# Performance work log

Hardware: AMD Instinct MI355X
Metric: run time of the kernel (lower is better)

Reference implementation:

```python
import jax, jax.numpy as jnp
import numpy as np

L, H, C, V, BLK = 6, 16, 1024, 32000, 2048
B, T, TA = 2, 512, 512
DFF = 4 * C
STD = 0.02
PROJ_STD = 0.02 / np.sqrt(2 * L)  # c_proj init per module
SCALE = 1.0 / np.sqrt(C // H)


def setup_inputs() -> dict:
    key = jax.random.key(0)
    ks = iter(jax.random.split(key, 64))
    nrm = lambda shape, std=STD: jax.random.normal(next(ks), shape, jnp.float32) * std
    inp = {
        'idx': jax.random.randint(next(ks), (B, T), 0, V),
        'xa': jax.random.normal(next(ks), (B, TA, C), jnp.float32),
        'wte': nrm((V, C)),            # tied with lm_head
        'wpe': nrm((BLK, C)),
        'ln1_w': jnp.ones((L, C)), 'ln1_b': jnp.zeros((L, C)),
        'sa_wq': nrm((L, C, C)), 'sa_bq': jnp.zeros((L, C)),
        'sa_wk': nrm((L, C, C)), 'sa_bk': jnp.zeros((L, C)),
        'sa_wv': nrm((L, C, C)), 'sa_bv': jnp.zeros((L, C)),
        'sa_wo': nrm((L, C, C), PROJ_STD), 'sa_bo': jnp.zeros((L, C)),
        'ca_wq': nrm((L, C, C)), 'ca_bq': jnp.zeros((L, C)),
        'ca_wk': nrm((L, C, C)), 'ca_bk': jnp.zeros((L, C)),
        'ca_wv': nrm((L, C, C)), 'ca_bv': jnp.zeros((L, C)),
        'ca_wo': nrm((L, C, C), PROJ_STD), 'ca_bo': jnp.zeros((L, C)),
        'ln2_w': jnp.ones((L, C)), 'ln2_b': jnp.zeros((L, C)),
        'fc_w': nrm((L, C, DFF)), 'fc_b': jnp.zeros((L, DFF)),
        'pr_w': nrm((L, DFF, C), PROJ_STD), 'pr_b': jnp.zeros((L, C)),
        'lnf_w': jnp.ones((C,)), 'lnf_b': jnp.zeros((C,)),
    }
    return inp


def _ln(h, w, b):
    m = h.mean(-1, keepdims=True)
    v = jnp.mean((h - m) ** 2, -1, keepdims=True)
    return (h - m) * jax.lax.rsqrt(v + 1e-5) * w + b


def _gelu(h):  # new_gelu (tanh approximation)
    return 0.5 * h * (1.0 + jnp.tanh(np.sqrt(2.0 / np.pi) * (h + 0.044715 * h ** 3)))


def _attn(hq, hkv, wq, bq, wk, bk, wv, bv, wo, bo):
    # NB: the original applies a tril causal mask even for cross-attention.
    Bq, Tq, _ = hq.shape
    Tk = hkv.shape[1]
    D = C // H
    q = (hq @ wq + bq).reshape(Bq, Tq, H, D)
    k = (hkv @ wk + bk).reshape(Bq, Tk, H, D)
    v = (hkv @ wv + bv).reshape(Bq, Tk, H, D)
    att = jnp.einsum('bqhd,bkhd->bhqk', q, k) * SCALE
    mask = jnp.tril(jnp.ones((Tq, Tk), bool))
    att = jnp.where(mask, att, -jnp.inf)
    att = jax.nn.softmax(att, axis=-1)
    y = jnp.einsum('bhqk,bkhd->bqhd', att, v).reshape(Bq, Tq, C)
    return y @ wo + bo


def _forward(idx, xa, wte, wpe, ln1_w, ln1_b, sa_wq, sa_bq, sa_wk, sa_bk, sa_wv, sa_bv, sa_wo, sa_bo,
             ca_wq, ca_bq, ca_wk, ca_bk, ca_wv, ca_bv, ca_wo, ca_bo,
             ln2_w, ln2_b, fc_w, fc_b, pr_w, pr_b, lnf_w, lnf_b):
    t = idx.shape[1]
    x = wte[idx] + wpe[:t][None]  # [B,T,C]

    def block(h, p):
        (l1w, l1b, sqw, sqb, skw, skb, svw, svb, sow, sob,
         cqw, cqb, ckw, ckb, cvw, cvb, cow, cob,
         l2w, l2b, fw, fb, pw, pb) = p
        n = _ln(h, l1w, l1b)
        h = h + _attn(n, n, sqw, sqb, skw, skb, svw, svb, sow, sob)
        n = _ln(h, l1w, l1b)  # ln_1 reused for cross-attn, as in source
        h = h + _attn(n, xa, cqw, cqb, ckw, ckb, cvw, cvb, cow, cob)
        n = _ln(h, l2w, l2b)
        h = h + (_gelu(n @ fw + fb) @ pw + pb)
        return h, None

    xs = (ln1_w, ln1_b, sa_wq, sa_bq, sa_wk, sa_bk, sa_wv, sa_bv, sa_wo, sa_bo,
          ca_wq, ca_bq, ca_wk, ca_bk, ca_wv, ca_bv, ca_wo, ca_bo,
          ln2_w, ln2_b, fc_w, fc_b, pr_w, pr_b)
    x, _ = jax.lax.scan(block, x, xs)
    x = _ln(x, lnf_w, lnf_b)
    return x @ wte.T  # tied lm_head, [B,T,V]


def reference(idx, xa, wte, wpe, ln1_w, ln1_b, sa_wq, sa_bq, sa_wk, sa_bk, sa_wv, sa_bv, sa_wo, sa_bo,
              ca_wq, ca_bq, ca_wk, ca_bk, ca_wv, ca_bv, ca_wo, ca_bo,
              ln2_w, ln2_b, fc_w, fc_b, pr_w, pr_b, lnf_w, lnf_b):
    return _forward(idx, xa, wte, wpe, ln1_w, ln1_b, sa_wq, sa_bq, sa_wk, sa_bk, sa_wv, sa_bv, sa_wo, sa_bo,
                    ca_wq, ca_bq, ca_wk, ca_bk, ca_wv, ca_bv, ca_wo, ca_bo,
                    ln2_w, ln2_b, fc_w, fc_b, pr_w, pr_b, lnf_w, lnf_b)
```

## Files before the change

kernel.cpp:

```cpp
#include <hip/hip_runtime.h>
#include <math.h>

#define CC   1024
#define HH   16
#define DH   64
#define TT   512
#define NTOK 1024
#define DFF_ 4096
#define VV   32000
#define QKSCALE 0.125f

typedef unsigned short u16;
typedef __attribute__((ext_vector_type(8))) short short8;
typedef __attribute__((ext_vector_type(4))) float f32x4;

__device__ __forceinline__ u16 f2bf(float f) {
  union { float f; unsigned u; } v; v.f = f;
  unsigned r = v.u + 0x7FFFu + ((v.u >> 16) & 1u);
  return (u16)(r >> 16);
}
__device__ __forceinline__ float gelu_f(float h) {
  return 0.5f * h * (1.0f + tanhf(0.7978845608028654f * (h + 0.044715f * h * h * h)));
}

template <int N> __device__ __forceinline__ void waitcnt_vm() {
  if constexpr (N == 0) asm volatile("s_waitcnt vmcnt(0)" ::: "memory");
  else if constexpr (N == 1) asm volatile("s_waitcnt vmcnt(1)" ::: "memory");
  else if constexpr (N == 2) asm volatile("s_waitcnt vmcnt(2)" ::: "memory");
  else if constexpr (N == 3) asm volatile("s_waitcnt vmcnt(3)" ::: "memory");
  else if constexpr (N == 4) asm volatile("s_waitcnt vmcnt(4)" ::: "memory");
  else if constexpr (N == 5) asm volatile("s_waitcnt vmcnt(5)" ::: "memory");
  else if constexpr (N == 6) asm volatile("s_waitcnt vmcnt(6)" ::: "memory");
  else if constexpr (N == 7) asm volatile("s_waitcnt vmcnt(7)" ::: "memory");
  else if constexpr (N == 8) asm volatile("s_waitcnt vmcnt(8)" ::: "memory");
  else static_assert(N <= 8, "unsupported vmcnt");
}

#define GLD16(gp, lp) __builtin_amdgcn_global_load_lds( \
    (const __attribute__((address_space(1))) void*)(gp), \
    (__attribute__((address_space(3))) void*)(lp), 16, 0, 0)

#define MFMA(a, b, c) __builtin_amdgcn_mfma_f32_16x16x32_bf16(a, b, c, 0, 0, 0)

__global__ __launch_bounds__(256) void embed_kernel(
    const int* __restrict__ idx, const float* __restrict__ wte,
    const float* __restrict__ wpe, float* __restrict__ x) {
  int row = blockIdx.x;
  int t = row & (TT - 1);
  int id = idx[row];
  const float4* a = (const float4*)(wte + (size_t)id * CC);
  const float4* p = (const float4*)(wpe + (size_t)t * CC);
  float4* o = (float4*)(x + (size_t)row * CC);
  int c = threadIdx.x;
  float4 va = a[c], vp = p[c];
  float4 ov;
  ov.x = va.x + vp.x; ov.y = va.y + vp.y; ov.z = va.z + vp.z; ov.w = va.w + vp.w;
  o[c] = ov;
}

__global__ __launch_bounds__(256) void ln_kernel(
    const float* __restrict__ x, const float* __restrict__ w,
    const float* __restrict__ b, u16* __restrict__ out) {
  int row = blockIdx.x, tid = threadIdx.x;
  float4 v = ((const float4*)(x + (size_t)row * CC))[tid];
  float s  = v.x + v.y + v.z + v.w;
  float sq = fmaf(v.x, v.x, fmaf(v.y, v.y, fmaf(v.z, v.z, v.w * v.w)));
  for (int o = 32; o > 0; o >>= 1) { s += __shfl_down(s, o); sq += __shfl_down(sq, o); }
  __shared__ float rs[4], rq[4];
  int wid = tid >> 6, lane = tid & 63;
  if (lane == 0) { rs[wid] = s; rq[wid] = sq; }
  __syncthreads();
  s  = rs[0] + rs[1] + rs[2] + rs[3];
  sq = rq[0] + rq[1] + rq[2] + rq[3];
  float mean = s * (1.0f / CC);
  float var  = sq * (1.0f / CC) - mean * mean;
  float rstd = 1.0f / sqrtf(var + 1e-5f);
  float4 wv = ((const float4*)w)[tid];
  float4 bv = ((const float4*)b)[tid];
  ushort4 o;
  o.x = f2bf((v.x - mean) * rstd * wv.x + bv.x);
  o.y = f2bf((v.y - mean) * rstd * wv.y + bv.y);
  o.z = f2bf((v.z - mean) * rstd * wv.z + bv.z);
  o.w = f2bf((v.w - mean) * rstd * wv.w + bv.w);
  ((ushort4*)(out + (size_t)row * CC))[tid] = o;
}

__global__ __launch_bounds__(256) void wtransL_kernel(
    const float* __restrict__ w0, const float* __restrict__ w1,
    const float* __restrict__ w2, const float* __restrict__ w3,
    const float* __restrict__ w4, const float* __restrict__ w5,
    const float* __restrict__ w6, const float* __restrict__ w7,
    const float* __restrict__ fc, const float* __restrict__ pr,
    u16* __restrict__ wt, size_t dls, int lbase) {
  const size_t M1 = 1048576;
  int z = blockIdx.z;
  int l = lbase + (z >> 4), slot = z & 15;
  size_t wofs = (size_t)l * M1;
  size_t mofs = (size_t)l * 4 * M1;
  const float* src;
  size_t doff = (size_t)(l - lbase) * dls;
  int sstr, dstr;
  if (slot < 8) {
    const float* base = slot == 0 ? w0 : slot == 1 ? w1 : slot == 2 ? w2
                      : slot == 3 ? w3 : slot == 4 ? w4 : slot == 5 ? w5
                      : slot == 6 ? w6 : w7;
    src = base + wofs; sstr = 1024; doff += (size_t)slot * M1; dstr = 1024;
  } else if (slot < 12) {
    int s = slot - 8;
    src = fc + mofs + (size_t)s * 1024; sstr = 4096;
    doff += 8 * M1 + (size_t)s * M1; dstr = 1024;
  } else {
    int s = slot - 12;
    src = pr + mofs + (size_t)s * M1; sstr = 1024;
    doff += 12 * M1 + (size_t)s * 1024; dstr = 4096;
  }
  __shared__ float t[64][65];
  int bx = blockIdx.x * 64, by = blockIdx.y * 64;
  int tid = threadIdx.x;
  int r16 = tid >> 4;
  int c4  = (tid & 15) * 4;
#pragma unroll
  for (int i = 0; i < 4; ++i) {
    int row = r16 + i * 16;
    float4 v = *(const float4*)&src[(size_t)(by + row) * sstr + bx + c4];
    t[row][c4] = v.x; t[row][c4 + 1] = v.y; t[row][c4 + 2] = v.z; t[row][c4 + 3] = v.w;
  }
  __syncthreads();
#pragma unroll
  for (int i = 0; i < 4; ++i) {
    int orow = r16 + i * 16;
    ushort4 o;
    o.x = f2bf(t[c4 + 0][orow]);
    o.y = f2bf(t[c4 + 1][orow]);
    o.z = f2bf(t[c4 + 2][orow]);
    o.w = f2bf(t[c4 + 3][orow]);
    *(ushort4*)&wt[doff + (size_t)(bx + orow) * dstr + by + c4] = o;
  }
}

__global__ __launch_bounds__(256) void convbf_kernel(
    const float* __restrict__ in, u16* __restrict__ out, int n4) {
  int i = blockIdx.x * 256 + threadIdx.x;
  if (i < n4) {
    float4 v = ((const float4*)in)[i];
    ushort4 o; o.x = f2bf(v.x); o.y = f2bf(v.y); o.z = f2bf(v.z); o.w = f2bf(v.w);
    ((ushort4*)out)[i] = o;
  }
}

template <int EPI, int MODE, int BM, int BN, int BK, int SK>
__global__ __launch_bounds__(256) void gemm_bf16_kernel(
    const u16* __restrict__ A, const u16* __restrict__ A2,
    const u16* __restrict__ B, const u16* __restrict__ B2,
    const float* __restrict__ bias, const float* __restrict__ bias2,
    const float* __restrict__ bias3, float* __restrict__ Cm,
    int K, int ldc, int whichbase) {
  constexpr int WM = BM / 2, WN = BN / 2, MF = WM / 16, NF = WN / 16;
  constexpr int KS = BK / 32;
  constexpr int NB = BK / 8;
  constexpr int PA = BM * BK / 2048;
  constexpr int PB = BN * BK / 2048;
  constexpr int RPP = 2048 / BK;
  constexpr int NBUF = (MODE == 2) ? 2 : 3;
  __shared__ u16 As[NBUF][BM * BK];
  __shared__ u16 Bs[NBUF][BN * BK];
  int tid = threadIdx.x;
  int lane = tid & 63, wave = tid >> 6;
  int wr = wave >> 1, wc = wave & 1;
  int row0, col0;
  bool isq = true;
  const u16* Ause = A;
  const u16* Buse = B;
  if (MODE == 2) {
    int id = blockIdx.x;
    int wg = (id & 7) * 250 + (id >> 3);
    row0 = (wg & 7) * BM;
    col0 = (wg >> 3) * BN;
  } else if (MODE == 3) {
    int bx = blockIdx.x;
    isq = bx < (1024 / BN);
    Ause = isq ? A : A2;
    Buse = isq ? B : B2;
    col0 = (isq ? bx : bx - 1024 / BN) * BN;
    row0 = blockIdx.y * BM;
  } else {
    row0 = blockIdx.y * BM;
    col0 = blockIdx.x * BN;
  }
  const int split = (SK > 1) ? blockIdx.z : 0;
  const int Kloc = K / SK;
  const int kbase = split * Kloc;
  f32x4 acc[MF][NF];
#pragma unroll
  for (int m = 0; m < MF; ++m)
#pragma unroll
    for (int n = 0; n < NF; ++n) acc[m][n] = (f32x4){0.f, 0.f, 0.f, 0.f};

  int srow = tid / NB;
  int sblk = (BK == 64) ? ((tid & 7) ^ ((tid >> 3) & 7))
                        : ((tid & 3) ^ ((tid >> 3) & 3));
  const u16* Ab = Ause + (size_t)row0 * K + kbase;
  int arow = wr * WM + (lane & 15);
  int brow = wc * WN + (lane & 15);
  int g8 = lane >> 4;
  const int NT = Kloc / BK;

  auto compute = [&](const u16* Ac, const u16* Bc) {
#pragma unroll
    for (int ks = 0; ks < KS; ++ks) {
      short8 af[MF], bg[NF];
#pragma unroll
      for (int m = 0; m < MF; ++m) {
        int row = arow + m * 16;
        int off = (BK == 64) ? row * 64 + (((ks * 4 + g8) ^ (row & 7)) << 3)
                             : row * 32 + ((g8 ^ ((row >> 1) & 3)) << 3);
        af[m] = *(const short8*)&Ac[off];
      }
#pragma unroll
      for (int n = 0; n < NF; ++n) {
        int row = brow + n * 16;
        int off = (BK == 64) ? row * 64 + (((ks * 4 + g8) ^ (row & 7)) << 3)
                             : row * 32 + ((g8 ^ ((row >> 1) & 3)) << 3);
        bg[n] = *(const short8*)&Bc[off];
      }
      __builtin_amdgcn_s_setprio(1);
#pragma unroll
      for (int m = 0; m < MF; ++m)
#pragma unroll
        for (int n = 0; n < NF; ++n)
          acc[m][n] = MFMA(af[m], bg[n], acc[m][n]);
      __builtin_amdgcn_s_setprio(0);
    }
  };

  if constexpr (MODE == 2) {
    const float* Bf = (const float*)B;
    int bsr = tid >> 2;
    int bkb = tid & 3;
    float4 rb0, rb1, rb2, rb3;
    auto loadB = [&](int k0) {
      const float* p0 = Bf + (size_t)(col0 + bsr) * 1024 + k0 + bkb * 8;
      const float* p1 = Bf + (size_t)(col0 + 64 + bsr) * 1024 + k0 + bkb * 8;
      rb0 = *(const float4*)p0; rb1 = *(const float4*)(p0 + 4);
      rb2 = *(const float4*)p1; rb3 = *(const float4*)(p1 + 4);
    };
    auto writeB = [&](int bufi) {
      u16 t0[8] = {f2bf(rb0.x), f2bf(rb0.y), f2bf(rb0.z), f2bf(rb0.w),
                   f2bf(rb1.x), f2bf(rb1.y), f2bf(rb1.z), f2bf(rb1.w)};
      u16 t1[8] = {f2bf(rb2.x), f2bf(rb2.y), f2bf(rb2.z), f2bf(rb2.w),
                   f2bf(rb3.x), f2bf(rb3.y), f2bf(rb3.z), f2bf(rb3.w)};
      int r1 = 64 + bsr;
      *(short8*)&Bs[bufi][bsr * 32 + ((bkb ^ ((bsr >> 1) & 3)) << 3)] = *(short8*)t0;
      *(short8*)&Bs[bufi][r1 * 32 + ((bkb ^ ((r1 >> 1) & 3)) << 3)] = *(short8*)t1;
    };
    auto stageA = [&](int bufi, int k0) {
#pragma unroll
      for (int p = 0; p < PA; ++p)
        GLD16(Ab + (size_t)(p * RPP + srow) * K + k0 + sblk * 8,
              &As[bufi][p * 2048 + wave * 512]);
    };
    loadB(0);
    stageA(0, 0);
    writeB(0);
    __syncthreads();
    for (int t = 0; t < NT; ++t) {
      int cur = t & 1;
      if (t + 1 < NT) { loadB((t + 1) * BK); stageA(cur ^ 1, (t + 1) * BK); }
      compute(As[cur], Bs[cur]);
      if (t + 1 < NT) writeB(cur ^ 1);
      __syncthreads();
    }
  } else {
    const u16* Bb = Buse + (size_t)col0 * K + kbase;
    auto stage = [&](int bufi, int k0) {
#pragma unroll
      for (int p = 0; p < PA; ++p)
        GLD16(Ab + (size_t)(p * RPP + srow) * K + k0 + sblk * 8,
              &As[bufi][p * 2048 + wave * 512]);
#pragma unroll
      for (int p = 0; p < PB; ++p)
        GLD16(Bb + (size_t)(p * RPP + srow) * K + k0 + sblk * 8,
              &Bs[bufi][p * 2048 + wave * 512]);
    };
    stage(0, 0);
    if (NT > 1) stage(1, BK);
    for (int t = 0; t < NT; ++t) {
      if (t + 1 < NT) waitcnt_vm<PA + PB>();
      else            waitcnt_vm<0>();
      __builtin_amdgcn_s_barrier();
      __builtin_amdgcn_sched_barrier(0);
      if (t + 2 < NT) stage((t + 2) % 3, (t + 2) * BK);
      int cur = t % 3;
      compute(As[cur], Bs[cur]);
    }
  }

  int r0 = row0 + wr * WM + g8 * 4;
  int c0 = col0 + wc * WN + (lane & 15);

  if (EPI == 4) {
    u16* qb = (u16*)Cm;
#pragma unroll
    for (int m = 0; m < MF; ++m)
#pragma unroll
      for (int n = 0; n < NF; ++n) {
        int j = c0 + n * 16;
        int which = (MODE == 3 ? (isq ? 0 : 1) : whichbase) + (j >> 10);
        const float* bp = which == 0 ? bias : (which == 1 ? bias2 : bias3);
        float bj = bp ? bp[j & 1023] : 0.0f;
        int h = (j & 1023) >> 6, d = j & 63;
        int trow0 = r0 + m * 16;
        int b = trow0 >> 9, t0 = trow0 & 511;
        int bh = b * 16 + h;
        u16 vals[4];
#pragma unroll
        for (int r = 0; r < 4; ++r) vals[r] = f2bf(acc[m][n][r] + bj);
        if (which < 2) {
          u16* dst = qb + (size_t)which * 1048576 + (size_t)bh * 32768 + (size_t)t0 * 64 + d;
#pragma unroll
          for (int r = 0; r < 4; ++r) dst[(size_t)r * 64] = vals[r];
        } else {
          u16* dst = qb + 2 * 1048576 + (size_t)bh * 32768 + (size_t)d * 512 + t0;
          *(ushort4*)dst = *(ushort4*)vals;
        }
      }
    return;
  }

  float bj[NF];
#pragma unroll
  for (int n = 0; n < NF; ++n)
    bj[n] = bias ? bias[c0 + n * 16] : 0.0f;
  u16* Cb = (u16*)Cm;
#pragma unroll
  for (int m = 0; m < MF; ++m)
#pragma unroll
    for (int n = 0; n < NF; ++n)
#pragma unroll
      for (int r = 0; r < 4; ++r) {
        size_t off = (size_t)(r0 + m * 16 + r) * ldc + c0 + n * 16;
        float v = acc[m][n][r] + ((SK == 1 || split == 0) ? bj[n] : 0.0f);
        if (EPI == 0) Cm[off] = v;
        else if (EPI == 1) {
          if constexpr (SK > 1) atomicAdd(&Cm[off], v);
          else Cm[off] += v;
        }
        else if (EPI == 2) Cb[off] = f2bf(gelu_f(v));
      }
}

__global__ __launch_bounds__(256) void attn_kernel(
    const u16* __restrict__ qh, const u16* __restrict__ kh,
    const u16* __restrict__ vt, u16* __restrict__ y) {
  __shared__ u16 P[32 * 512];
  __shared__ float smax[4][32], ssum[4][32];
  int tid = threadIdx.x, lane = tid & 63, w = tid >> 6;
  int bx = blockIdx.x, bh = blockIdx.y;
  int q0 = bx * 32;
  int b = bh >> 4, h = bh & 15;
  const u16* qb = qh + (size_t)bh * 32768;
  const u16* kb = kh + (size_t)bh * 32768;
  const u16* vb = vt + (size_t)bh * 32768;
  int g = lane >> 4, c = lane & 15;

  short8 a[2][2];
#pragma unroll
  for (int rt = 0; rt < 2; ++rt)
#pragma unroll
    for (int ks = 0; ks < 2; ++ks)
      a[rt][ks] = *(const short8*)(qb + (size_t)(q0 + rt * 16 + c) * 64 + ks * 32 + g * 8);

  int lim = q0 + 31;
  int nct = (lim - w * 128) / 16 + 1;
  if (nct > 8) nct = 8;
  if (nct < 0) nct = 0;
  f32x4 s[2][8];
#pragma unroll
  for (int rt = 0; rt < 2; ++rt)
#pragma unroll
    for (int ct = 0; ct < 8; ++ct) s[rt][ct] = (f32x4){0.f, 0.f, 0.f, 0.f};
  for (int ct = 0; ct < nct; ++ct) {
    int n0 = w * 128 + ct * 16;
#pragma unroll
    for (int ks = 0; ks < 2; ++ks) {
      short8 bf = *(const short8*)(kb + (size_t)(n0 + c) * 64 + ks * 32 + g * 8);
      s[0][ct] = MFMA(a[0][ks], bf, s[0][ct]);
      s[1][ct] = MFMA(a[1][ks], bf, s[1][ct]);
    }
  }

  float mx[2][4];
#pragma unroll
  for (int rt = 0; rt < 2; ++rt)
#pragma unroll
    for (int r = 0; r < 4; ++r) mx[rt][r] = -1e30f;
  for (int ct = 0; ct < nct; ++ct) {
    int col = w * 128 + ct * 16 + c;
#pragma unroll
    for (int rt = 0; rt < 2; ++rt)
#pragma unroll
      for (int r = 0; r < 4; ++r) {
        int trow = q0 + rt * 16 + g * 4 + r;
        float v = s[rt][ct][r] * QKSCALE;
        if (col > trow) v = -1e30f;
        s[rt][ct][r] = v;
        mx[rt][r] = fmaxf(mx[rt][r], v);
      }
  }
#pragma unroll
  for (int off = 1; off < 16; off <<= 1)
#pragma unroll
    for (int rt = 0; rt < 2; ++rt)
#pragma unroll
      for (int r = 0; r < 4; ++r) mx[rt][r] = fmaxf(mx[rt][r], __shfl_xor(mx[rt][r], off));
  if (c == 0)
#pragma unroll
    for (int rt = 0; rt < 2; ++rt)
#pragma unroll
      for (int r = 0; r < 4; ++r) smax[w][rt * 16 + g * 4 + r] = mx[rt][r];
  __syncthreads();

  float m_[2][4], sum[2][4];
#pragma unroll
  for (int rt = 0; rt < 2; ++rt)
#pragma unroll
    for (int r = 0; r < 4; ++r) {
      int row = rt * 16 + g * 4 + r;
      m_[rt][r] = fmaxf(fmaxf(smax[0][row], smax[1][row]), fmaxf(smax[2][row], smax[3][row]));
      sum[rt][r] = 0.f;
    }
  for (int ct = 0; ct < nct; ++ct) {
    int col = w * 128 + ct * 16 + c;
    int blk = col >> 3, cl = col & 7;
#pragma unroll
    for (int rt = 0; rt < 2; ++rt)
#pragma unroll
      for (int r = 0; r < 4; ++r) {
        float p = __expf(s[rt][ct][r] - m_[rt][r]);
        sum[rt][r] += p;
        int row = rt * 16 + g * 4 + r;
        int hsh = (row ^ (row >> 2)) & 7;
        P[row * 512 + ((blk ^ hsh) << 3) + cl] = f2bf(p);
      }
  }
#pragma unroll
  for (int off = 1; off < 16; off <<= 1)
#pragma unroll
    for (int rt = 0; rt < 2; ++rt)
#pragma unroll
      for (int r = 0; r < 4; ++r) sum[rt][r] += __shfl_xor(sum[rt][r], off);
  if (c == 0)
#pragma unroll
    for (int rt = 0; rt < 2; ++rt)
#pragma unroll
      for (int r = 0; r < 4; ++r) ssum[w][rt * 16 + g * 4 + r] = sum[rt][r];
  __syncthreads();

  float li[2][4];
#pragma unroll
  for (int rt = 0; rt < 2; ++rt)
#pragma unroll
    for (int r = 0; r < 4; ++r) {
      int row = rt * 16 + g * 4 + r;
      li[rt][r] = 1.0f / (ssum[0][row] + ssum[1][row] + ssum[2][row] + ssum[3][row]);
    }

  int rt2 = w >> 1, nh = w & 1;
  f32x4 o[2];
  o[0] = (f32x4){0.f, 0.f, 0.f, 0.f};
  o[1] = (f32x4){0.f, 0.f, 0.f, 0.f};
  int nks = bx + 1;
  int prow = rt2 * 16 + c;
  int phsh = (prow ^ (prow >> 2)) & 7;
  for (int ks = 0; ks < nks; ++ks) {
    short8 pa = *(const short8*)&P[prow * 512 + (((ks * 4 + g) ^ phsh) << 3)];
#pragma unroll
    for (int nt = 0; nt < 2; ++nt) {
      int d = nh * 32 + nt * 16 + c;
      short8 vf = *(const short8*)(vb + (size_t)d * 512 + ks * 32 + g * 8);
      o[nt] = MFMA(pa, vf, o[nt]);
    }
  }
#pragma unroll
  for (int nt = 0; nt < 2; ++nt)
#pragma unroll
    for (int r = 0; r < 4; ++r) {
      int trow = q0 + rt2 * 16 + g * 4 + r;
      float val = o[nt][r] * li[rt2][r];
      y[(size_t)(b * 512 + trow) * 1024 + h * 64 + nh * 32 + nt * 16 + c] = f2bf(val);
    }
}

extern "C" void kernel_launch(void* const* d_in, const int* in_sizes, int n_in,
                              void* d_out, int out_size, void* d_ws, size_t ws_size,
                              hipStream_t stream) {
  const int*   idx   = (const int*)d_in[0];
  const float* xa    = (const float*)d_in[1];
  const float* wte   = (const float*)d_in[2];
  const float* wpe   = (const float*)d_in[3];
  const float* ln1_w = (const float*)d_in[4];
  const float* ln1_b = (const float*)d_in[5];
  const float* sa_wq = (const float*)d_in[6];
  const float* sa_bq = (const float*)d_in[7];
  const float* sa_wk = (const float*)d_in[8];
  const float* sa_bk = (const float*)d_in[9];
  const float* sa_wv = (const float*)d_in[10];
  const float* sa_bv = (const float*)d_in[11];
  const float* sa_wo = (const float*)d_in[12];
  const float* sa_bo = (const float*)d_in[13];
  const float* ca_wq = (const float*)d_in[14];
  const float* ca_bq = (const float*)d_in[15];
  const float* ca_wk = (const float*)d_in[16];
  const float* ca_bk = (const float*)d_in[17];
  const float* ca_wv = (const float*)d_in[18];
  const float* ca_bv = (const float*)d_in[19];
  const float* ca_wo = (const float*)d_in[20];
  const float* ca_bo = (const float*)d_in[21];
  const float* ln2_w = (const float*)d_in[22];
  const float* ln2_b = (const float*)d_in[23];
  const float* fc_w  = (const float*)d_in[24];
  const float* fc_b  = (const float*)d_in[25];
  const float* pr_w  = (const float*)d_in[26];
  const float* pr_b  = (const float*)d_in[27];
  const float* lnf_w = (const float*)d_in[28];
  const float* lnf_b = (const float*)d_in[29];

  const size_t M1 = 1048576;
  float* ws     = (float*)d_ws;
  float* x      = ws;
  u16* qkvh  = (u16*)(x + M1);
  u16* nbf   = qkvh + 3 * M1;
  u16* ybf   = nbf + M1;
  u16* hmbf  = ybf + M1;
  u16* xabf  = hmbf + 4 * M1;
  u16* wT    = xabf + M1;

  const bool full = ws_size >= 226492416ull;
  const size_t wls = full ? 16 * M1 : 0;

  const size_t oQKV = 0, oWO = 3 * M1, oCQ = 4 * M1, oCKV = 5 * M1,
               oCWO = 7 * M1, oFC = 8 * M1, oPR = 12 * M1;

  embed_kernel<<<NTOK, 256, 0, stream>>>(idx, wte, wpe, x);
  convbf_kernel<<<(NTOK * CC / 4 + 255) / 256, 256, 0, stream>>>(xa, xabf, NTOK * CC / 4);
  if (full)
    wtransL_kernel<<<dim3(16, 16, 96), 256, 0, stream>>>(
        sa_wq, sa_wk, sa_wv, sa_wo, ca_wq, ca_wk, ca_wv, ca_wo,
        fc_w, pr_w, wT, wls, 0);

  for (int l = 0; l < 6; ++l) {
    size_t bofs = (size_t)l * CC;
    u16* wTl = wT + (size_t)l * wls;

    if (!full)
      wtransL_kernel<<<dim3(16, 16, 16), 256, 0, stream>>>(
          sa_wq, sa_wk, sa_wv, sa_wo, ca_wq, ca_wk, ca_wv, ca_wo,
          fc_w, pr_w, wT, 0, l);

    ln_kernel<<<NTOK, 256, 0, stream>>>(x, ln1_w + bofs, ln1_b + bofs, nbf);
    gemm_bf16_kernel<4, 0, 64, 128, 64, 1><<<dim3(24, 16), 256, 0, stream>>>(
        nbf, nullptr, wTl + oQKV, nullptr, sa_bq + bofs, sa_bk + bofs,
        sa_bv + bofs, (float*)qkvh, CC, 0, 0);
    attn_kernel<<<dim3(16, 32), 256, 0, stream>>>(qkvh, qkvh + M1, qkvh + 2 * M1, ybf);
    gemm_bf16_kernel<1, 0, 32, 64, 64, 2><<<dim3(16, 32, 2), 256, 0, stream>>>(
        ybf, nullptr, wTl + oWO, nullptr, sa_bo + bofs, nullptr, nullptr,
        x, CC, CC, 0);

    ln_kernel<<<NTOK, 256, 0, stream>>>(x, ln1_w + bofs, ln1_b + bofs, nbf);
    gemm_bf16_kernel<4, 3, 64, 64, 64, 1><<<dim3(48, 16), 256, 0, stream>>>(
        nbf, xabf, wTl + oCQ, wTl + oCKV, ca_bq + bofs, ca_bk + bofs,
        ca_bv + bofs, (float*)qkvh, CC, 0, 0);
    attn_kernel<<<dim3(16, 32), 256, 0, stream>>>(qkvh, qkvh + M1, qkvh + 2 * M1, ybf);
    gemm_bf16_kernel<1, 0, 32, 64, 64, 2><<<dim3(16, 32, 2), 256, 0, stream>>>(
        ybf, nullptr, wTl + oCWO, nullptr, ca_bo + bofs, nullptr, nullptr,
        x, CC, CC, 0);

    ln_kernel<<<NTOK, 256, 0, stream>>>(x, ln2_w + bofs, ln2_b + bofs, nbf);
    gemm_bf16_kernel<2, 0, 64, 128, 64, 1><<<dim3(32, 16), 256, 0, stream>>>(
        nbf, nullptr, wTl + oFC, nullptr, fc_b + (size_t)l * DFF_, nullptr,
        nullptr, (float*)hmbf, CC, DFF_, 0);
    gemm_bf16_kernel<1, 0, 32, 64, 64, 4><<<dim3(16, 32, 4), 256, 0, stream>>>(
        hmbf, nullptr, wTl + oPR, nullptr, pr_b + bofs, nullptr, nullptr,
        x, DFF_, CC, 0);
  }

  ln_kernel<<<NTOK, 256, 0, stream>>>(x, lnf_w, lnf_b, nbf);
  gemm_bf16_kernel<0, 2, 128, 128, 32, 1><<<dim3(2000), 256, 0, stream>>>(
      nbf, nullptr, (const u16*)wte, nullptr, nullptr, nullptr, nullptr,
      (float*)d_out, CC, VV, 0);
}
```

Before: 1.516 ms.

## Pre-convert tied wte to bf16 and add single-buffer bf16 lm_head GEMM mode

New measurement: 1.509 ms. Within noise of the previous version (-0.5%).

```diff
diff --git a/kernel.cpp b/kernel.cpp
--- a/kernel.cpp
+++ b/kernel.cpp
@@ -161,7 +161,7 @@
   constexpr int PA = BM * BK / 2048;
   constexpr int PB = BN * BK / 2048;
   constexpr int RPP = 2048 / BK;
-  constexpr int NBUF = (MODE == 2) ? 2 : 3;
+  constexpr int NBUF = (MODE == 2) ? 2 : (MODE == 4 ? 1 : 3);
   __shared__ u16 As[NBUF][BM * BK];
   __shared__ u16 Bs[NBUF][BN * BK];
   int tid = threadIdx.x;
@@ -171,7 +171,7 @@
   bool isq = true;
   const u16* Ause = A;
   const u16* Buse = B;
-  if (MODE == 2) {
+  if (MODE == 2 || MODE == 4) {
     int id = blockIdx.x;
     int wg = (id & 7) * 250 + (id >> 3);
     row0 = (wg & 7) * BM;
@@ -268,6 +268,22 @@
       if (t + 1 < NT) { loadB((t + 1) * BK); stageA(cur ^ 1, (t + 1) * BK); }
       compute(As[cur], Bs[cur]);
       if (t + 1 < NT) writeB(cur ^ 1);
+      __syncthreads();
+    }
+  } else if constexpr (MODE == 4) {
+    const u16* Bb = Buse + (size_t)col0 * K + kbase;
+    for (int t = 0; t < NT; ++t) {
+      int k0 = t * BK;
+#pragma unroll
+      for (int p = 0; p < PA; ++p)
+        GLD16(Ab + (size_t)(p * RPP + srow) * K + k0 + sblk * 8,
+              &As[0][p * 2048 + wave * 512]);
+#pragma unroll
+      for (int p = 0; p < PB; ++p)
+        GLD16(Bb + (size_t)(p * RPP + srow) * K + k0 + sblk * 8,
+              &Bs[0][p * 2048 + wave * 512]);
+      __syncthreads();
+      compute(As[0], Bs[0]);
       __syncthreads();
     }
   } else {
@@ -533,9 +549,11 @@
   u16* ybf   = nbf + M1;
   u16* hmbf  = ybf + M1;
   u16* xabf  = hmbf + 4 * M1;
-  u16* wT    = xabf + M1;
-
-  const bool full = ws_size >= 226492416ull;
+
+  const bool fullW = ws_size >= 292028416ull;
+  const bool full  = fullW || ws_size >= 226492416ull;
+  u16* wtebf = xabf + M1;
+  u16* wT    = fullW ? wtebf + (size_t)VV * CC : xabf + M1;
   const size_t wls = full ? 16 * M1 : 0;
 
   const size_t oQKV = 0, oWO = 3 * M1, oCQ = 4 * M1, oCKV = 5 * M1,
@@ -543,6 +561,8 @@
 
   embed_kernel<<<NTOK, 256, 0, stream>>>(idx, wte, wpe, x);
   convbf_kernel<<<(NTOK * CC / 4 + 255) / 256, 256, 0, stream>>>(xa, xabf, NTOK * CC / 4);
+  if (fullW)
+    convbf_kernel<<<(VV * CC / 4 + 255) / 256, 256, 0, stream>>>(wte, wtebf, VV * CC / 4);
   if (full)
     wtransL_kernel<<<dim3(16, 16, 96), 256, 0, stream>>>(
         sa_wq, sa_wk, sa_wv, sa_wo, ca_wq, ca_wk, ca_wv, ca_wo,
@@ -585,7 +605,12 @@
   }
 
   ln_kernel<<<NTOK, 256, 0, stream>>>(x, lnf_w, lnf_b, nbf);
-  gemm_bf16_kernel<0, 2, 128, 128, 32, 1><<<dim3(2000), 256, 0, stream>>>(
-      nbf, nullptr, (const u16*)wte, nullptr, nullptr, nullptr, nullptr,
-      (float*)d_out, CC, VV, 0);
-}
+  if (fullW)
+    gemm_bf16_kernel<0, 4, 128, 128, 64, 1><<<dim3(2000), 256, 0, stream>>>(
+        nbf, nullptr, wtebf, nullptr, nullptr, nullptr, nullptr,
+        (float*)d_out, CC, VV, 0);
+  else
+    gemm_bf16_kernel<0, 2, 128, 128, 32, 1><<<dim3(2000), 256, 0, stream>>>(
+        nbf, nullptr, (const u16*)wte, nullptr, nullptr, nullptr, nullptr,
+        (float*)d_out, CC, VV, 0);
+}
```
